# Kernel optimization log

Measured on AMD Instinct MI355X. Metric: run time of the kernel, lower is better.

The kernel has to match this reference:

```python
import jax, jax.numpy as jnp
import numpy as np

D = 512
H = 8
DH = D // H
EPS = 1e-5


def _layernorm(x, g, b):
    mu = jnp.mean(x, axis=-1, keepdims=True)
    var = jnp.mean((x - mu) ** 2, axis=-1, keepdims=True)
    return (x - mu) * jax.lax.rsqrt(var + EPS) * g + b


def setup_inputs() -> dict:
    key = jax.random.key(0)
    ks = jax.random.split(key, 10)
    B, S = 4, 2048
    s = 1.0 / np.sqrt(D)
    return {
        "x": jax.random.normal(ks[0], (B, S, D), dtype=jnp.float32),
        "Wq": jax.random.normal(ks[1], (D, D), dtype=jnp.float32) * s,
        "Wk": jax.random.normal(ks[2], (D, D), dtype=jnp.float32) * s,
        "Wv": jax.random.normal(ks[3], (D, D), dtype=jnp.float32) * s,
        "Wo": jax.random.normal(ks[4], (D, D), dtype=jnp.float32) * s,
        "W1": jax.random.normal(ks[5], (4 * D, D), dtype=jnp.float32) * s,
        "b1": jnp.zeros((4 * D,), dtype=jnp.float32),
        "W2": jax.random.normal(ks[6], (D, 4 * D), dtype=jnp.float32) * (1.0 / np.sqrt(4 * D)),
        "b2": jnp.zeros((D,), dtype=jnp.float32),
        "g1": jnp.ones((D,), dtype=jnp.float32),
        "bb1": jnp.zeros((D,), dtype=jnp.float32),
        "g2": jnp.ones((D,), dtype=jnp.float32),
        "bb2": jnp.zeros((D,), dtype=jnp.float32),
    }


def reference(x, Wq, Wk, Wv, Wo, W1, b1, W2, b2, g1, bb1, g2, bb2):
    B, S, _ = x.shape
    # projections (torch Linear: y = x @ W.T), split heads: chunk(-1) == reshape to [B,S,H,DH]
    q = (x @ Wq.T).reshape(B, S, H, DH).transpose(0, 2, 1, 3)  # [B,H,S,DH]
    k = (x @ Wk.T).reshape(B, S, H, DH).transpose(0, 2, 1, 3)
    v = (x @ Wv.T).reshape(B, S, H, DH).transpose(0, 2, 1, 3)
    scores = jnp.einsum("bhsd,bhtd->bhst", q, k) / np.sqrt(DH)  # [B,H,S,S]
    attn = jax.nn.softmax(scores, axis=-1)
    ctx = jnp.einsum("bhst,bhtd->bhsd", attn, v)  # [B,H,S,DH]
    ctx = ctx.transpose(0, 2, 1, 3).reshape(B, S, D)
    h = _layernorm(x + ctx @ Wo.T, g1, bb1)
    mlp = jax.nn.relu(h @ W1.T + b1) @ W2.T + b2
    return _layernorm(h + mlp, g2, bb2)
```

## Files before the change

### kernel.cpp

```cpp
#include <hip/hip_runtime.h>
#include <hip/hip_bf16.h>
#include <cstdint>
#include <cstddef>

typedef short bf16x8 __attribute__((ext_vector_type(8)));
typedef float floatx4 __attribute__((ext_vector_type(4)));
typedef unsigned short u16;

constexpr int B = 4, S = 2048, D = 512, H = 8, DH = 64;
constexpr int M_ROWS = B * S;
constexpr int D4 = 4 * D;
constexpr float QSCALE = 0.18033688011112042f;

__device__ __forceinline__ u16 f2b(float f) {
  unsigned u = __builtin_bit_cast(unsigned, f);
  u += 0x7fff + ((u >> 16) & 1);
  return (u16)(u >> 16);
}

__device__ __forceinline__ bf16x8 ldfrag(const u16* p) {
  return *reinterpret_cast<const bf16x8*>(p);
}

__device__ __forceinline__ floatx4 mfma16(bf16x8 a, bf16x8 b, floatx4 c) {
  return __builtin_amdgcn_mfma_f32_16x16x32_bf16(a, b, c, 0, 0, 0);
}

__device__ __forceinline__ ushort4 f2b4(float4 v) {
  ushort4 r;
  r.x = f2b(v.x); r.y = f2b(v.y); r.z = f2b(v.z); r.w = f2b(v.w);
  return r;
}

__device__ __forceinline__ void gld16(const u16* g, u16* l) {
  __builtin_amdgcn_global_load_lds(
      (const __attribute__((address_space(1))) void*)g,
      (__attribute__((address_space(3))) void*)l, 16, 0, 0);
}

__global__ void cast4_kernel(const float4* __restrict__ in, ushort4* __restrict__ out, int n4) {
  int i = blockIdx.x * blockDim.x + threadIdx.x;
  if (i < n4) out[i] = f2b4(in[i]);
}

__global__ void cast_w_kernel(const float4* __restrict__ w1, const float4* __restrict__ w2,
                              const float4* __restrict__ wq, const float4* __restrict__ wk,
                              const float4* __restrict__ wv, const float4* __restrict__ wo,
                              ushort4* __restrict__ w1b, ushort4* __restrict__ w2b,
                              ushort4* __restrict__ wqb, ushort4* __restrict__ wkb,
                              ushort4* __restrict__ wvb, ushort4* __restrict__ wob) {
  int i = blockIdx.x * blockDim.x + threadIdx.x;
  constexpr int N1 = (D4 * D) / 4;
  constexpr int NS = (D * D) / 4;
  if (i < N1) { w1b[i] = f2b4(w1[i]); return; }
  i -= N1;
  if (i < N1) { w2b[i] = f2b4(w2[i]); return; }
  i -= N1;
  const int sel = i >> 16, off = i & (NS - 1);
  const float4* src = sel == 0 ? wq : sel == 1 ? wk : sel == 2 ? wv : wo;
  ushort4* dst = sel == 0 ? wqb : sel == 1 ? wkb : sel == 2 ? wvb : wob;
  dst[off] = f2b4(src[off]);
}

template <int EPI>
__global__ __launch_bounds__(256) void gemm_bt(
    const u16* __restrict__ A, const u16* __restrict__ W,
    const float* __restrict__ bias, void* __restrict__ out0, void* __restrict__ out1,
    int M, int N, int K, int klen) {
  __shared__ __align__(16) u16 As[2][128 * 32];
  __shared__ __align__(16) u16 Bs[2][128 * 32];
  const int wave = threadIdx.x >> 6, lane = threadIdx.x & 63;
  const int quad = lane >> 4, l16 = lane & 15;
  const int rowB = blockIdx.y * 128, colB = blockIdx.x * 128;
  const int rowW = (wave >> 1) * 64, colW = (wave & 1) * 64;
  const int koff = blockIdx.z * klen;
  void* out = blockIdx.z ? out1 : out0;

  floatx4 acc[4][4];
#pragma unroll
  for (int i = 0; i < 4; i++)
#pragma unroll
    for (int j = 0; j < 4; j++) acc[i][j] = (floatx4){0.f,0.f,0.f,0.f};

  const u16* gA = A + (size_t)(rowB + wave * 32 + (lane >> 2)) * K + koff + (lane & 3) * 8;
  const u16* gB = W + (size_t)(colB + wave * 32 + (lane >> 2)) * K + koff + (lane & 3) * 8;
  const int lds_off = wave * 1024;

#pragma unroll
  for (int rr = 0; rr < 2; rr++) {
    gld16(gA + (size_t)rr * 16 * K, &As[0][lds_off + rr * 512]);
    gld16(gB + (size_t)rr * 16 * K, &Bs[0][lds_off + rr * 512]);
  }

  int buf = 0;
  for (int kc = 0; kc < klen; kc += 32, buf ^= 1) {
    __syncthreads();

    if (kc + 32 < klen) {
#pragma unroll
      for (int rr = 0; rr < 2; rr++) {
        gld16(gA + (size_t)rr * 16 * K + kc + 32, &As[buf ^ 1][lds_off + rr * 512]);
        gld16(gB + (size_t)rr * 16 * K + kc + 32, &Bs[buf ^ 1][lds_off + rr * 512]);
      }
    }

    bf16x8 a[4], b[4];
#pragma unroll
    for (int i = 0; i < 4; i++)
      a[i] = ldfrag(&As[buf][(rowW + i * 16 + l16) * 32 + quad * 8]);
#pragma unroll
    for (int j = 0; j < 4; j++)
      b[j] = ldfrag(&Bs[buf][(colW + j * 16 + l16) * 32 + quad * 8]);
#pragma unroll
    for (int i = 0; i < 4; i++)
#pragma unroll
      for (int j = 0; j < 4; j++) acc[i][j] = mfma16(a[i], b[j], acc[i][j]);
  }

#pragma unroll
  for (int i = 0; i < 4; i++) {
#pragma unroll
    for (int j = 0; j < 4; j++) {
      const int gn = colB + colW + j * 16 + l16;
      const float bv = (EPI == 1) ? bias[gn] : 0.f;
#pragma unroll
      for (int r = 0; r < 4; r++) {
        const int gm = rowB + rowW + i * 16 + quad * 4 + r;
        float v = acc[i][j][r] + bv;
        if (EPI == 0) {
          ((float*)out)[(size_t)gm * N + gn] = v;
        } else {
          v = v > 0.f ? v : 0.f;
          ((u16*)out)[(size_t)gm * N + gn] = f2b(v);
        }
      }
    }
  }
}

__global__ __launch_bounds__(256) void qkv_gemm(
    const u16* __restrict__ xb,
    const u16* __restrict__ wq, const u16* __restrict__ wk, const u16* __restrict__ wv,
    u16* __restrict__ q, u16* __restrict__ k, u16* __restrict__ vT) {
  __shared__ __align__(16) u16 As[2][128 * 32];
  __shared__ __align__(16) u16 Bs[2][128 * 32];
  const int which = blockIdx.z;
  const u16* __restrict__ W = which == 0 ? wq : (which == 1 ? wk : wv);
  const int wave = threadIdx.x >> 6, lane = threadIdx.x & 63;
  const int quad = lane >> 4, l16 = lane & 15;
  const int rowB = blockIdx.y * 128, colB = blockIdx.x * 128;
  const int rowW = (wave >> 1) * 64, colW = (wave & 1) * 64;

  floatx4 acc[4][4];
#pragma unroll
  for (int i = 0; i < 4; i++)
#pragma unroll
    for (int j = 0; j < 4; j++) acc[i][j] = (floatx4){0.f,0.f,0.f,0.f};

  const u16* gA = xb + (size_t)(rowB + wave * 32 + (lane >> 2)) * D + (lane & 3) * 8;
  const u16* gB = W + (size_t)(colB + wave * 32 + (lane >> 2)) * D + (lane & 3) * 8;
  const int lds_off = wave * 1024;

#pragma unroll
  for (int rr = 0; rr < 2; rr++) {
    gld16(gA + (size_t)rr * 16 * D, &As[0][lds_off + rr * 512]);
    gld16(gB + (size_t)rr * 16 * D, &Bs[0][lds_off + rr * 512]);
  }

  int buf = 0;
  for (int kc = 0; kc < D; kc += 32, buf ^= 1) {
    __syncthreads();

    if (kc + 32 < D) {
#pragma unroll
      for (int rr = 0; rr < 2; rr++) {
        gld16(gA + (size_t)rr * 16 * D + kc + 32, &As[buf ^ 1][lds_off + rr * 512]);
        gld16(gB + (size_t)rr * 16 * D + kc + 32, &Bs[buf ^ 1][lds_off + rr * 512]);
      }
    }

    bf16x8 a[4], b[4];
#pragma unroll
    for (int i = 0; i < 4; i++)
      a[i] = ldfrag(&As[buf][(rowW + i * 16 + l16) * 32 + quad * 8]);
#pragma unroll
    for (int j = 0; j < 4; j++)
      b[j] = ldfrag(&Bs[buf][(colW + j * 16 + l16) * 32 + quad * 8]);
#pragma unroll
    for (int i = 0; i < 4; i++)
#pragma unroll
      for (int j = 0; j < 4; j++) acc[i][j] = mfma16(a[i], b[j], acc[i][j]);
  }

  const float oscale = (which == 0) ? QSCALE : 1.0f;
  u16* dst01 = which == 0 ? q : k;
#pragma unroll
  for (int i = 0; i < 4; i++) {
#pragma unroll
    for (int j = 0; j < 4; j++) {
      const int gn = colB + colW + j * 16 + l16;
      const int h = gn >> 6, dh = gn & 63;
#pragma unroll
      for (int r = 0; r < 4; r++) {
        const int gm = rowB + rowW + i * 16 + quad * 4 + r;
        const int bb = gm >> 11, s = gm & 2047;
        const u16 val = f2b(acc[i][j][r] * oscale);
        if (which < 2) {
          dst01[((((size_t)bb * H + h) * S) + s) * DH + dh] = val;
        } else {
          vT[((((size_t)bb * H + h) * DH) + dh) * S + s] = val;
        }
      }
    }
  }
}

constexpr int PST = 72;

__global__ __launch_bounds__(256, 1) void attn_kernel(
    const u16* __restrict__ q, const u16* __restrict__ k,
    const u16* __restrict__ vT, u16* __restrict__ ctxb) {
  __shared__ __align__(16) u16 kvlds[2][2][2][64 * 32];
  __shared__ __align__(16) u16 plds[4][64 * PST];
  __shared__ float lb[4][64];
  const int wave = threadIdx.x >> 6, lane = threadIdx.x & 63;
  const int quad = lane >> 4, l16 = lane & 15;
  const int blk = (blockIdx.x & 7) * 32 + (blockIdx.x >> 3);
  const int w = blk * 4 + wave;
  const int bh = w >> 5, qt = w & 31;
  const int bb = bh >> 3, h = bh & 7;

  const u16* qp = q + ((size_t)bh * S + qt * 64 + l16) * DH + quad * 8;
  bf16x8 qf[4][2];
#pragma unroll
  for (int t = 0; t < 4; t++) {
    qf[t][0] = ldfrag(qp + (size_t)t * 16 * DH);
    qf[t][1] = ldfrag(qp + (size_t)t * 16 * DH + 32);
  }

  const int st = threadIdx.x;
  const int srow = st >> 2, sp = (st & 3) * 8;
  const u16* kS = k + (size_t)bh * S * DH + (size_t)srow * DH + sp;
  const u16* vS = vT + (size_t)bh * DH * S + (size_t)srow * S + sp;

  floatx4 o[4][4];
#pragma unroll
  for (int t = 0; t < 4; t++)
#pragma unroll
    for (int c = 0; c < 4; c++) o[t][c] = (floatx4){0.f,0.f,0.f,0.f};
  float lacc[4] = {0.f, 0.f, 0.f, 0.f};

  u16* myp = plds[wave];
  u16* wpb = myp + l16 * PST + quad * 4;
  const u16* rpb = myp + l16 * PST + quad * 8;

  {
    gld16(kS, &kvlds[0][0][0][wave * 512]);
    gld16(kS + 32, &kvlds[0][0][1][wave * 512]);
    gld16(vS, &kvlds[0][1][0][wave * 512]);
    gld16(vS + 32, &kvlds[0][1][1][wave * 512]);
  }

  int buf = 0;
  for (int kt = 0; kt < S; kt += 64, buf ^= 1) {
    __syncthreads();

    bf16x8 kf[8], vf[8];
#pragma unroll
    for (int i = 0; i < 4; i++) {
      kf[2 * i]     = ldfrag(&kvlds[buf][0][0][(i * 16 + l16) * 32 + quad * 8]);
      kf[2 * i + 1] = ldfrag(&kvlds[buf][0][1][(i * 16 + l16) * 32 + quad * 8]);
      vf[2 * i]     = ldfrag(&kvlds[buf][1][0][(i * 16 + l16) * 32 + quad * 8]);
      vf[2 * i + 1] = ldfrag(&kvlds[buf][1][1][(i * 16 + l16) * 32 + quad * 8]);
    }

    if (kt + 64 < S) {
      const int nb = buf ^ 1;
      gld16(kS + (size_t)(kt + 64) * DH, &kvlds[nb][0][0][wave * 512]);
      gld16(kS + (size_t)(kt + 64) * DH + 32, &kvlds[nb][0][1][wave * 512]);
      gld16(vS + kt + 64, &kvlds[nb][1][0][wave * 512]);
      gld16(vS + kt + 96, &kvlds[nb][1][1][wave * 512]);
    }

#pragma unroll
    for (int t = 0; t < 4; t++) {
      floatx4 sc[4];
#pragma unroll
      for (int i = 0; i < 4; i++) {
        floatx4 z = (floatx4){0.f,0.f,0.f,0.f};
        z = mfma16(kf[2 * i], qf[t][0], z);
        z = mfma16(kf[2 * i + 1], qf[t][1], z);
        sc[i] = z;
      }
      float a = 0.f;
#pragma unroll
      for (int i = 0; i < 4; i++) {
        const float p0 = __builtin_amdgcn_exp2f(sc[i][0]);
        const float p1 = __builtin_amdgcn_exp2f(sc[i][1]);
        const float p2 = __builtin_amdgcn_exp2f(sc[i][2]);
        const float p3 = __builtin_amdgcn_exp2f(sc[i][3]);
        a += (p0 + p1) + (p2 + p3);
        ushort4 pk = {f2b(p0), f2b(p1), f2b(p2), f2b(p3)};
        *reinterpret_cast<ushort4*>(&wpb[t * 16 * PST + i * 16]) = pk;
      }
      lacc[t] += a;
    }

#pragma unroll
    for (int t = 0; t < 4; t++) {
      const bf16x8 pf0 = ldfrag(rpb + (size_t)t * 16 * PST);
      const bf16x8 pf1 = ldfrag(rpb + (size_t)t * 16 * PST + 32);
#pragma unroll
      for (int c = 0; c < 4; c++) {
        o[t][c] = mfma16(pf0, vf[2 * c], o[t][c]);
        o[t][c] = mfma16(pf1, vf[2 * c + 1], o[t][c]);
      }
    }
  }

  float lt[4];
#pragma unroll
  for (int t = 0; t < 4; t++) {
    float l = lacc[t];
    l += __shfl_xor(l, 16);
    l += __shfl_xor(l, 32);
    lt[t] = l;
  }
  if (quad == 0) {
#pragma unroll
    for (int t = 0; t < 4; t++) lb[wave][t * 16 + l16] = lt[t];
  }
  __builtin_amdgcn_wave_barrier();
  float inv[4][4];
#pragma unroll
  for (int t = 0; t < 4; t++)
#pragma unroll
    for (int r = 0; r < 4; r++)
      inv[t][r] = 1.0f / lb[wave][t * 16 + quad * 4 + r];

  const size_t crow_base = ((size_t)bb * S) * D + h * DH;
#pragma unroll
  for (int t = 0; t < 4; t++)
#pragma unroll
    for (int c = 0; c < 4; c++) {
      const int dh = c * 16 + l16;
#pragma unroll
      for (int r = 0; r < 4; r++) {
        const int s = qt * 64 + t * 16 + quad * 4 + r;
        ctxb[crow_base + (size_t)s * D + dh] = f2b(o[t][c][r] * inv[t][r]);
      }
    }
}

template <bool BF16OUT, bool PB>
__global__ __launch_bounds__(256) void ln_kernel(
    const float* __restrict__ resid, const float* __restrict__ ya,
    const float* __restrict__ yb, const float* __restrict__ pb,
    const float* __restrict__ g, const float* __restrict__ bvec,
    float* __restrict__ outF, u16* __restrict__ outB) {
  const int wave = threadIdx.x >> 6, lane = threadIdx.x & 63;
  const int row = blockIdx.x * 4 + wave;
  const float* rp = resid + (size_t)row * D + lane * 8;
  const float* ap = ya + (size_t)row * D + lane * 8;
  const float* bp = yb + (size_t)row * D + lane * 8;
  float v[8];
  const float4 r0 = *(const float4*)rp, r1 = *(const float4*)(rp + 4);
  const float4 a0 = *(const float4*)ap, a1 = *(const float4*)(ap + 4);
  const float4 b0 = *(const float4*)bp, b1 = *(const float4*)(bp + 4);
  v[0] = r0.x + a0.x + b0.x; v[1] = r0.y + a0.y + b0.y;
  v[2] = r0.z + a0.z + b0.z; v[3] = r0.w + a0.w + b0.w;
  v[4] = r1.x + a1.x + b1.x; v[5] = r1.y + a1.y + b1.y;
  v[6] = r1.z + a1.z + b1.z; v[7] = r1.w + a1.w + b1.w;
  if (PB) {
    const float4 p0 = *(const float4*)(pb + lane * 8);
    const float4 p1 = *(const float4*)(pb + lane * 8 + 4);
    v[0] += p0.x; v[1] += p0.y; v[2] += p0.z; v[3] += p0.w;
    v[4] += p1.x; v[5] += p1.y; v[6] += p1.z; v[7] += p1.w;
  }
  float sum = 0.f;
#pragma unroll
  for (int i = 0; i < 8; i++) sum += v[i];
#pragma unroll
  for (int d = 1; d < 64; d <<= 1) sum += __shfl_xor(sum, d);
  const float mu = sum * (1.f / D);
  float vs = 0.f;
#pragma unroll
  for (int i = 0; i < 8; i++) { const float t = v[i] - mu; vs += t * t; }
#pragma unroll
  for (int d = 1; d < 64; d <<= 1) vs += __shfl_xor(vs, d);
  const float rstd = rsqrtf(vs * (1.f / D) + 1e-5f);
#pragma unroll
  for (int i = 0; i < 8; i++) {
    const int col = lane * 8 + i;
    const float o = (v[i] - mu) * rstd * g[col] + bvec[col];
    outF[(size_t)row * D + col] = o;
    if (BF16OUT) outB[(size_t)row * D + col] = f2b(o);
  }
}

constexpr size_t OFF_XB  = 0;
constexpr size_t OFF_WQB = 8u << 20;
constexpr size_t OFF_WKB = OFF_WQB + (512u << 10);
constexpr size_t OFF_WVB = OFF_WKB + (512u << 10);
constexpr size_t OFF_WOB = OFF_WVB + (512u << 10);
constexpr size_t OFF_W1B = 10u << 20;
constexpr size_t OFF_W2B = 12u << 20;
constexpr size_t OFF_Q   = 14u << 20;
constexpr size_t OFF_K   = 22u << 20;
constexpr size_t OFF_VT  = 30u << 20;
constexpr size_t OFF_CTX = 38u << 20;
constexpr size_t OFF_Y   = 46u << 20;
constexpr size_t OFF_H   = 62u << 20;
constexpr size_t OFF_HB  = 78u << 20;
constexpr size_t OFF_M1B = 86u << 20;

extern "C" void kernel_launch(void* const* d_in, const int* in_sizes, int n_in,
                              void* d_out, int out_size, void* d_ws, size_t ws_size,
                              hipStream_t stream) {
  const float* x  = (const float*)d_in[0];
  const float* Wq = (const float*)d_in[1];
  const float* Wk = (const float*)d_in[2];
  const float* Wv = (const float*)d_in[3];
  const float* Wo = (const float*)d_in[4];
  const float* W1 = (const float*)d_in[5];
  const float* b1 = (const float*)d_in[6];
  const float* W2 = (const float*)d_in[7];
  const float* b2 = (const float*)d_in[8];
  const float* g1 = (const float*)d_in[9];
  const float* bb1 = (const float*)d_in[10];
  const float* g2 = (const float*)d_in[11];
  const float* bb2 = (const float*)d_in[12];

  char* ws = (char*)d_ws;
  u16* xb  = (u16*)(ws + OFF_XB);
  u16* wqb = (u16*)(ws + OFF_WQB);
  u16* wkb = (u16*)(ws + OFF_WKB);
  u16* wvb = (u16*)(ws + OFF_WVB);
  u16* wob = (u16*)(ws + OFF_WOB);
  u16* w1b = (u16*)(ws + OFF_W1B);
  u16* w2b = (u16*)(ws + OFF_W2B);
  u16* qb  = (u16*)(ws + OFF_Q);
  u16* kb  = (u16*)(ws + OFF_K);
  u16* vtb = (u16*)(ws + OFF_VT);
  u16* ctxb = (u16*)(ws + OFF_CTX);
  float* y0 = (float*)(ws + OFF_Y);
  float* y1 = (float*)(ws + OFF_Q);
  float* hf = (float*)(ws + OFF_H);
  u16* hb  = (u16*)(ws + OFF_HB);
  u16* m1b = (u16*)(ws + OFF_M1B);

  cast4_kernel<<<(M_ROWS * D / 4 + 255) / 256, 256, 0, stream>>>(
      (const float4*)x, (ushort4*)xb, M_ROWS * D / 4);
  {
    const int n4 = (D4 * D) / 4 * 2 + (D * D) / 4 * 4;
    cast_w_kernel<<<(n4 + 255) / 256, 256, 0, stream>>>(
        (const float4*)W1, (const float4*)W2, (const float4*)Wq, (const float4*)Wk,
        (const float4*)Wv, (const float4*)Wo,
        (ushort4*)w1b, (ushort4*)w2b, (ushort4*)wqb, (ushort4*)wkb,
        (ushort4*)wvb, (ushort4*)wob);
  }

  qkv_gemm<<<dim3(D / 128, M_ROWS / 128, 3), 256, 0, stream>>>(xb, wqb, wkb, wvb, qb, kb, vtb);

  attn_kernel<<<B * H * S / 64 / 4, 256, 0, stream>>>(qb, kb, vtb, ctxb);

  gemm_bt<0><<<dim3(D / 128, M_ROWS / 128, 2), 256, 0, stream>>>(
      ctxb, wob, nullptr, y0, y1, M_ROWS, D, D, D / 2);

  ln_kernel<true, false><<<M_ROWS / 4, 256, 0, stream>>>(
      x, y0, y1, nullptr, g1, bb1, hf, hb);

  gemm_bt<1><<<dim3(D4 / 128, M_ROWS / 128, 1), 256, 0, stream>>>(
      hb, w1b, b1, m1b, nullptr, M_ROWS, D4, D, D);

  gemm_bt<0><<<dim3(D / 128, M_ROWS / 128, 2), 256, 0, stream>>>(
      m1b, w2b, nullptr, y0, y1, M_ROWS, D, D4, D4 / 2);

  ln_kernel<false, true><<<M_ROWS / 4, 256, 0, stream>>>(
      hf, y0, y1, b2, g2, bb2, (float*)d_out, nullptr);
}
```

Baseline: 277.6 us.

## Split attention keys across wave pairs, fuse cast kernels, drop fp32 LN residual

The attention kernel now runs 512 threads per block, with two waves per query tile each covering half of the key sequence. The partial outputs and row sums are merged through LDS at the end, which doubles the parallelism per tile and halves the serial key loop. The casts of x and the weights are merged into one launch. The second layernorm now reads the bf16 copy of h instead of an fp32 copy, cutting a full fp32 write and read. The fp32-to-bf16 rounding of P changes to a cheaper add-and-perm, and reading h in bf16 loses residual precision.

```diff
diff --git a/kernel.cpp b/kernel.cpp
--- a/kernel.cpp
+++ b/kernel.cpp
@@ -38,20 +38,20 @@
       (__attribute__((address_space(3))) void*)l, 16, 0, 0);
 }
 
-__global__ void cast4_kernel(const float4* __restrict__ in, ushort4* __restrict__ out, int n4) {
+__global__ void cast_all_kernel(const float4* __restrict__ x,
+                                const float4* __restrict__ w1, const float4* __restrict__ w2,
+                                const float4* __restrict__ wq, const float4* __restrict__ wk,
+                                const float4* __restrict__ wv, const float4* __restrict__ wo,
+                                ushort4* __restrict__ xb,
+                                ushort4* __restrict__ w1b, ushort4* __restrict__ w2b,
+                                ushort4* __restrict__ wqb, ushort4* __restrict__ wkb,
+                                ushort4* __restrict__ wvb, ushort4* __restrict__ wob) {
   int i = blockIdx.x * blockDim.x + threadIdx.x;
-  if (i < n4) out[i] = f2b4(in[i]);
-}
-
-__global__ void cast_w_kernel(const float4* __restrict__ w1, const float4* __restrict__ w2,
-                              const float4* __restrict__ wq, const float4* __restrict__ wk,
-                              const float4* __restrict__ wv, const float4* __restrict__ wo,
-                              ushort4* __restrict__ w1b, ushort4* __restrict__ w2b,
-                              ushort4* __restrict__ wqb, ushort4* __restrict__ wkb,
-                              ushort4* __restrict__ wvb, ushort4* __restrict__ wob) {
-  int i = blockIdx.x * blockDim.x + threadIdx.x;
+  constexpr int NX = (M_ROWS * D) / 4;
   constexpr int N1 = (D4 * D) / 4;
   constexpr int NS = (D * D) / 4;
+  if (i < NX) { xb[i] = f2b4(x[i]); return; }
+  i -= NX;
   if (i < N1) { w1b[i] = f2b4(w1[i]); return; }
   i -= N1;
   if (i < N1) { w2b[i] = f2b4(w2[i]); return; }
@@ -217,16 +217,16 @@
 
 constexpr int PST = 72;
 
-__global__ __launch_bounds__(256, 1) void attn_kernel(
+__global__ __launch_bounds__(512, 1) void attn_kernel(
     const u16* __restrict__ q, const u16* __restrict__ k,
     const u16* __restrict__ vT, u16* __restrict__ ctxb) {
-  __shared__ __align__(16) u16 kvlds[2][2][2][64 * 32];
-  __shared__ __align__(16) u16 plds[4][64 * PST];
-  __shared__ float lb[4][64];
+  __shared__ __align__(16) u16 kvlds[2][2][2][2][64 * 32];
+  __shared__ __align__(16) u16 plds[8][64 * PST];
   const int wave = threadIdx.x >> 6, lane = threadIdx.x & 63;
   const int quad = lane >> 4, l16 = lane & 15;
+  const int pair = wave >> 1, khalf = wave & 1;
   const int blk = (blockIdx.x & 7) * 32 + (blockIdx.x >> 3);
-  const int w = blk * 4 + wave;
+  const int w = blk * 4 + pair;
   const int bh = w >> 5, qt = w & 31;
   const int bb = bh >> 3, h = bh & 7;
 
@@ -238,10 +238,10 @@
     qf[t][1] = ldfrag(qp + (size_t)t * 16 * DH + 32);
   }
 
-  const int st = threadIdx.x;
+  const int st = pair * 64 + lane;
   const int srow = st >> 2, sp = (st & 3) * 8;
-  const u16* kS = k + (size_t)bh * S * DH + (size_t)srow * DH + sp;
-  const u16* vS = vT + (size_t)bh * DH * S + (size_t)srow * S + sp;
+  const u16* kS = k + (size_t)bh * S * DH + (size_t)(khalf * 1024 + srow) * DH + sp;
+  const u16* vS = vT + (size_t)bh * DH * S + (size_t)srow * S + khalf * 1024 + sp;
 
   floatx4 o[4][4];
 #pragma unroll
@@ -254,32 +254,30 @@
   u16* wpb = myp + l16 * PST + quad * 4;
   const u16* rpb = myp + l16 * PST + quad * 8;
 
-  {
-    gld16(kS, &kvlds[0][0][0][wave * 512]);
-    gld16(kS + 32, &kvlds[0][0][1][wave * 512]);
-    gld16(vS, &kvlds[0][1][0][wave * 512]);
-    gld16(vS + 32, &kvlds[0][1][1][wave * 512]);
-  }
+  gld16(kS, &kvlds[0][khalf][0][0][pair * 512]);
+  gld16(kS + 32, &kvlds[0][khalf][0][1][pair * 512]);
+  gld16(vS, &kvlds[0][khalf][1][0][pair * 512]);
+  gld16(vS + 32, &kvlds[0][khalf][1][1][pair * 512]);
 
   int buf = 0;
-  for (int kt = 0; kt < S; kt += 64, buf ^= 1) {
+  for (int kt = 0; kt < S / 2; kt += 64, buf ^= 1) {
     __syncthreads();
 
     bf16x8 kf[8], vf[8];
 #pragma unroll
     for (int i = 0; i < 4; i++) {
-      kf[2 * i]     = ldfrag(&kvlds[buf][0][0][(i * 16 + l16) * 32 + quad * 8]);
-      kf[2 * i + 1] = ldfrag(&kvlds[buf][0][1][(i * 16 + l16) * 32 + quad * 8]);
-      vf[2 * i]     = ldfrag(&kvlds[buf][1][0][(i * 16 + l16) * 32 + quad * 8]);
-      vf[2 * i + 1] = ldfrag(&kvlds[buf][1][1][(i * 16 + l16) * 32 + quad * 8]);
-    }
-
-    if (kt + 64 < S) {
+      kf[2 * i]     = ldfrag(&kvlds[buf][khalf][0][0][(i * 16 + l16) * 32 + quad * 8]);
+      kf[2 * i + 1] = ldfrag(&kvlds[buf][khalf][0][1][(i * 16 + l16) * 32 + quad * 8]);
+      vf[2 * i]     = ldfrag(&kvlds[buf][khalf][1][0][(i * 16 + l16) * 32 + quad * 8]);
+      vf[2 * i + 1] = ldfrag(&kvlds[buf][khalf][1][1][(i * 16 + l16) * 32 + quad * 8]);
+    }
+
+    if (kt + 64 < S / 2) {
       const int nb = buf ^ 1;
-      gld16(kS + (size_t)(kt + 64) * DH, &kvlds[nb][0][0][wave * 512]);
-      gld16(kS + (size_t)(kt + 64) * DH + 32, &kvlds[nb][0][1][wave * 512]);
-      gld16(vS + kt + 64, &kvlds[nb][1][0][wave * 512]);
-      gld16(vS + kt + 96, &kvlds[nb][1][1][wave * 512]);
+      gld16(kS + (size_t)(kt + 64) * DH, &kvlds[nb][khalf][0][0][pair * 512]);
+      gld16(kS + (size_t)(kt + 64) * DH + 32, &kvlds[nb][khalf][0][1][pair * 512]);
+      gld16(vS + kt + 64, &kvlds[nb][khalf][1][0][pair * 512]);
+      gld16(vS + kt + 96, &kvlds[nb][khalf][1][1][pair * 512]);
     }
 
 #pragma unroll
@@ -300,8 +298,14 @@
         const float p2 = __builtin_amdgcn_exp2f(sc[i][2]);
         const float p3 = __builtin_amdgcn_exp2f(sc[i][3]);
         a += (p0 + p1) + (p2 + p3);
-        ushort4 pk = {f2b(p0), f2b(p1), f2b(p2), f2b(p3)};
-        *reinterpret_cast<ushort4*>(&wpb[t * 16 * PST + i * 16]) = pk;
+        const unsigned lo = __builtin_amdgcn_perm(
+            __builtin_bit_cast(unsigned, p1) + 0x8000u,
+            __builtin_bit_cast(unsigned, p0) + 0x8000u, 0x07060302u);
+        const unsigned hi = __builtin_amdgcn_perm(
+            __builtin_bit_cast(unsigned, p3) + 0x8000u,
+            __builtin_bit_cast(unsigned, p2) + 0x8000u, 0x07060302u);
+        uint2 pk; pk.x = lo; pk.y = hi;
+        *reinterpret_cast<uint2*>(&wpb[t * 16 * PST + i * 16]) = pk;
       }
       lacc[t] += a;
     }
@@ -326,52 +330,81 @@
     l += __shfl_xor(l, 32);
     lt[t] = l;
   }
+
+  float* ob = reinterpret_cast<float*>(plds[2 * pair]);
+  float* lb0 = ob + 64 * 64;
+  float* lb1 = lb0 + 64;
+
+  __syncthreads();
   if (quad == 0) {
-#pragma unroll
-    for (int t = 0; t < 4; t++) lb[wave][t * 16 + l16] = lt[t];
-  }
-  __builtin_amdgcn_wave_barrier();
-  float inv[4][4];
-#pragma unroll
-  for (int t = 0; t < 4; t++)
-#pragma unroll
-    for (int r = 0; r < 4; r++)
-      inv[t][r] = 1.0f / lb[wave][t * 16 + quad * 4 + r];
-
-  const size_t crow_base = ((size_t)bb * S) * D + h * DH;
-#pragma unroll
-  for (int t = 0; t < 4; t++)
-#pragma unroll
-    for (int c = 0; c < 4; c++) {
-      const int dh = c * 16 + l16;
-#pragma unroll
-      for (int r = 0; r < 4; r++) {
-        const int s = qt * 64 + t * 16 + quad * 4 + r;
-        ctxb[crow_base + (size_t)s * D + dh] = f2b(o[t][c][r] * inv[t][r]);
-      }
-    }
-}
-
-template <bool BF16OUT, bool PB>
+    float* dst = khalf ? lb1 : lb0;
+#pragma unroll
+    for (int t = 0; t < 4; t++) dst[t * 16 + l16] = lt[t];
+  }
+  if (khalf == 1) {
+#pragma unroll
+    for (int t = 0; t < 4; t++)
+#pragma unroll
+      for (int c = 0; c < 4; c++)
+        *reinterpret_cast<floatx4*>(&ob[lane * 64 + (t * 4 + c) * 4]) = o[t][c];
+  }
+  __syncthreads();
+  if (khalf == 0) {
+    float inv[4][4];
+#pragma unroll
+    for (int t = 0; t < 4; t++)
+#pragma unroll
+      for (int r = 0; r < 4; r++)
+        inv[t][r] = 1.0f / (lb0[t * 16 + quad * 4 + r] + lb1[t * 16 + quad * 4 + r]);
+
+    const size_t crow_base = ((size_t)bb * S) * D + h * DH;
+#pragma unroll
+    for (int t = 0; t < 4; t++)
+#pragma unroll
+      for (int c = 0; c < 4; c++) {
+        const floatx4 oo = o[t][c] +
+            *reinterpret_cast<const floatx4*>(&ob[lane * 64 + (t * 4 + c) * 4]);
+        const int dh = c * 16 + l16;
+#pragma unroll
+        for (int r = 0; r < 4; r++) {
+          const int s = qt * 64 + t * 16 + quad * 4 + r;
+          ctxb[crow_base + (size_t)s * D + dh] = f2b(oo[r] * inv[t][r]);
+        }
+      }
+  }
+}
+
+template <int MODE>
 __global__ __launch_bounds__(256) void ln_kernel(
-    const float* __restrict__ resid, const float* __restrict__ ya,
+    const void* __restrict__ resid, const float* __restrict__ ya,
     const float* __restrict__ yb, const float* __restrict__ pb,
     const float* __restrict__ g, const float* __restrict__ bvec,
     float* __restrict__ outF, u16* __restrict__ outB) {
   const int wave = threadIdx.x >> 6, lane = threadIdx.x & 63;
   const int row = blockIdx.x * 4 + wave;
-  const float* rp = resid + (size_t)row * D + lane * 8;
   const float* ap = ya + (size_t)row * D + lane * 8;
   const float* bp = yb + (size_t)row * D + lane * 8;
   float v[8];
-  const float4 r0 = *(const float4*)rp, r1 = *(const float4*)(rp + 4);
   const float4 a0 = *(const float4*)ap, a1 = *(const float4*)(ap + 4);
   const float4 b0 = *(const float4*)bp, b1 = *(const float4*)(bp + 4);
-  v[0] = r0.x + a0.x + b0.x; v[1] = r0.y + a0.y + b0.y;
-  v[2] = r0.z + a0.z + b0.z; v[3] = r0.w + a0.w + b0.w;
-  v[4] = r1.x + a1.x + b1.x; v[5] = r1.y + a1.y + b1.y;
-  v[6] = r1.z + a1.z + b1.z; v[7] = r1.w + a1.w + b1.w;
-  if (PB) {
+  v[0] = a0.x + b0.x; v[1] = a0.y + b0.y; v[2] = a0.z + b0.z; v[3] = a0.w + b0.w;
+  v[4] = a1.x + b1.x; v[5] = a1.y + b1.y; v[6] = a1.z + b1.z; v[7] = a1.w + b1.w;
+  if (MODE == 0) {
+    const float* rp = (const float*)resid + (size_t)row * D + lane * 8;
+    const float4 r0 = *(const float4*)rp, r1 = *(const float4*)(rp + 4);
+    v[0] += r0.x; v[1] += r0.y; v[2] += r0.z; v[3] += r0.w;
+    v[4] += r1.x; v[5] += r1.y; v[6] += r1.z; v[7] += r1.w;
+  } else {
+    const u16* rp = (const u16*)resid + (size_t)row * D + lane * 8;
+    const ushort4 h0 = *(const ushort4*)rp, h1 = *(const ushort4*)(rp + 4);
+    v[0] += __builtin_bit_cast(float, (unsigned)h0.x << 16);
+    v[1] += __builtin_bit_cast(float, (unsigned)h0.y << 16);
+    v[2] += __builtin_bit_cast(float, (unsigned)h0.z << 16);
+    v[3] += __builtin_bit_cast(float, (unsigned)h0.w << 16);
+    v[4] += __builtin_bit_cast(float, (unsigned)h1.x << 16);
+    v[5] += __builtin_bit_cast(float, (unsigned)h1.y << 16);
+    v[6] += __builtin_bit_cast(float, (unsigned)h1.z << 16);
+    v[7] += __builtin_bit_cast(float, (unsigned)h1.w << 16);
     const float4 p0 = *(const float4*)(pb + lane * 8);
     const float4 p1 = *(const float4*)(pb + lane * 8 + 4);
     v[0] += p0.x; v[1] += p0.y; v[2] += p0.z; v[3] += p0.w;
@@ -393,8 +426,8 @@
   for (int i = 0; i < 8; i++) {
     const int col = lane * 8 + i;
     const float o = (v[i] - mu) * rstd * g[col] + bvec[col];
-    outF[(size_t)row * D + col] = o;
-    if (BF16OUT) outB[(size_t)row * D + col] = f2b(o);
+    if (MODE == 0) outB[(size_t)row * D + col] = f2b(o);
+    else           outF[(size_t)row * D + col] = o;
   }
 }
 
@@ -410,7 +443,6 @@
 constexpr size_t OFF_VT  = 30u << 20;
 constexpr size_t OFF_CTX = 38u << 20;
 constexpr size_t OFF_Y   = 46u << 20;
-constexpr size_t OFF_H   = 62u << 20;
 constexpr size_t OFF_HB  = 78u << 20;
 constexpr size_t OFF_M1B = 86u << 20;
 
@@ -445,30 +477,27 @@
   u16* ctxb = (u16*)(ws + OFF_CTX);
   float* y0 = (float*)(ws + OFF_Y);
   float* y1 = (float*)(ws + OFF_Q);
-  float* hf = (float*)(ws + OFF_H);
   u16* hb  = (u16*)(ws + OFF_HB);
   u16* m1b = (u16*)(ws + OFF_M1B);
 
-  cast4_kernel<<<(M_ROWS * D / 4 + 255) / 256, 256, 0, stream>>>(
-      (const float4*)x, (ushort4*)xb, M_ROWS * D / 4);
   {
-    const int n4 = (D4 * D) / 4 * 2 + (D * D) / 4 * 4;
-    cast_w_kernel<<<(n4 + 255) / 256, 256, 0, stream>>>(
-        (const float4*)W1, (const float4*)W2, (const float4*)Wq, (const float4*)Wk,
-        (const float4*)Wv, (const float4*)Wo,
-        (ushort4*)w1b, (ushort4*)w2b, (ushort4*)wqb, (ushort4*)wkb,
-        (ushort4*)wvb, (ushort4*)wob);
+    const int n4 = (M_ROWS * D) / 4 + (D4 * D) / 4 * 2 + (D * D) / 4 * 4;
+    cast_all_kernel<<<(n4 + 255) / 256, 256, 0, stream>>>(
+        (const float4*)x, (const float4*)W1, (const float4*)W2, (const float4*)Wq,
+        (const float4*)Wk, (const float4*)Wv, (const float4*)Wo,
+        (ushort4*)xb, (ushort4*)w1b, (ushort4*)w2b, (ushort4*)wqb,
+        (ushort4*)wkb, (ushort4*)wvb, (ushort4*)wob);
   }
 
   qkv_gemm<<<dim3(D / 128, M_ROWS / 128, 3), 256, 0, stream>>>(xb, wqb, wkb, wvb, qb, kb, vtb);
 
-  attn_kernel<<<B * H * S / 64 / 4, 256, 0, stream>>>(qb, kb, vtb, ctxb);
+  attn_kernel<<<B * H * S / 64 / 4, 512, 0, stream>>>(qb, kb, vtb, ctxb);
 
   gemm_bt<0><<<dim3(D / 128, M_ROWS / 128, 2), 256, 0, stream>>>(
       ctxb, wob, nullptr, y0, y1, M_ROWS, D, D, D / 2);
 
-  ln_kernel<true, false><<<M_ROWS / 4, 256, 0, stream>>>(
-      x, y0, y1, nullptr, g1, bb1, hf, hb);
+  ln_kernel<0><<<M_ROWS / 4, 256, 0, stream>>>(
+      x, y0, y1, nullptr, g1, bb1, nullptr, hb);
 
   gemm_bt<1><<<dim3(D4 / 128, M_ROWS / 128, 1), 256, 0, stream>>>(
       hb, w1b, b1, m1b, nullptr, M_ROWS, D4, D, D);
@@ -476,6 +505,6 @@
   gemm_bt<0><<<dim3(D / 128, M_ROWS / 128, 2), 256, 0, stream>>>(
       m1b, w2b, nullptr, y0, y1, M_ROWS, D, D4, D4 / 2);
 
-  ln_kernel<false, true><<<M_ROWS / 4, 256, 0, stream>>>(
-      hf, y0, y1, b2, g2, bb2, (float*)d_out, nullptr);
-}
+  ln_kernel<1><<<M_ROWS / 4, 256, 0, stream>>>(
+      hb, y0, y1, b2, g2, bb2, (float*)d_out, nullptr);
+}
```

Result: faster. 261.3 us (-5.8%).
